# Optimization experiments

Measured on AMD Instinct MI355X. Metric: run time of the kernel, lower is better.

## Reference

```python
import jax, jax.numpy as jnp
import numpy as np

N = 64
DX0 = np.pi / N
B = 4096
N_ENV = 8
CODE = 128


def setup_inputs() -> dict:
    key = jax.random.key(0)
    k1, k2, k3 = jax.random.split(key, 3)
    y0 = jax.random.normal(k1, (B, 1, N, N), dtype=jnp.float32)
    env = jax.random.randint(k2, (B,), 0, N_ENV).astype(jnp.int64)
    codes = jax.random.normal(k3, (B, CODE), dtype=jnp.float32)
    t = jnp.zeros((1,), dtype=jnp.float32)
    # learned params: [mu, domain_placeholder] per env (matches nn.Parameter init)
    params = jnp.concatenate([jnp.full((N_ENV, 1), 0.005, jnp.float32),
                              jnp.full((N_ENV, 1), 1.0, jnp.float32)], axis=1)
    # fixed domain buffer for n_env == 8
    domain = jnp.array([0.75, 1.0, 0.75, 1.0, 0.75, 1.0, 0.75, 1.0],
                       dtype=jnp.float32)[:, None]  # [n_env, 1]
    return {"t": t, "y0": y0, "env": env, "codes": codes,
            "params": params, "domain": domain}


def _dx(a):  # roll along last axis (torch dims=2 on [B,H,W])
    return jnp.roll(a, -1, axis=2) - jnp.roll(a, 1, axis=2)


def _dy(a):  # roll along axis 1
    return jnp.roll(a, -1, axis=1) - jnp.roll(a, 1, axis=1)


def _laplacian2d(a, fdx2):
    # torch conv2d (cross-correlation) with kernel [[0,1,0],[1,-4,1],[1,1,0]]
    # and circular padding; note the asymmetric bottom row (faithful to source).
    lap = (jnp.roll(a, 1, axis=1)                    # a[i-1, j]
           + jnp.roll(a, 1, axis=2)                  # a[i, j-1]
           - 4.0 * a
           + jnp.roll(a, -1, axis=2)                 # a[i, j+1]
           + jnp.roll(jnp.roll(a, -1, axis=1), 1, axis=2)  # a[i+1, j-1]
           + jnp.roll(a, -1, axis=1))                # a[i+1, j]
    return lap / fdx2


def _poisson_solve(w, fdx):
    # w: [B,N,N]; fdx: [B,1] grid spacing per sample
    w_pad = jnp.pad(w, ((0, 0), (0, 1), (0, 1)), mode='wrap')  # [B,N+1,N+1]
    wf = jnp.fft.fft2(w_pad / (N ** 2))
    base = jnp.fft.fftfreq(N + 1).astype(w.dtype)       # fftfreq(n, d) = base / d
    k = (2.0 * np.pi) * base[None, :] / fdx             # [B, N+1]
    k2 = k[:, :, None] ** 2 + k[:, None, :] ** 2        # [B, N+1, N+1]
    uf = -wf / (1e-12 + k2)
    uf = uf.at[:, 0, 0].set(0.0)
    return jnp.fft.ifft2((N ** 2) * uf).real[:, :N, :N]


def reference(t, y0, env, codes, params, domain):
    x = y0[:, 0]                              # [B,N,N]
    p = params[env]                           # [B,2]
    mu = p[:, 0:1][..., None]                 # [B,1,1]
    fdx = domain[env] * DX0                   # [B,1]
    psi = _poisson_solve(-x, fdx)             # [B,N,N]
    fdx2 = (fdx[..., None]) ** 2              # [B,1,1]

    rxm = jnp.roll(x, -1, axis=2); rxp = jnp.roll(x, 1, axis=2)
    rym = jnp.roll(x, -1, axis=1); ryp = jnp.roll(x, 1, axis=1)
    pxm = jnp.roll(psi, -1, axis=2); pxp = jnp.roll(psi, 1, axis=2)
    pym = jnp.roll(psi, -1, axis=1); pyp = jnp.roll(psi, 1, axis=1)

    J1 = (_dy(psi) * _dx(x) - _dx(psi) * _dy(x)) / (4.0 * fdx2)
    J2 = (rxm * _dy(pxm) - rxp * _dy(pxp)
          - rym * _dx(pym) + ryp * _dx(pyp)) / (4.0 * fdx2)
    J3 = (jnp.roll(rxm, -1, axis=1) * (pym - pxm)
          - jnp.roll(rxp, 1, axis=1) * (pxp - pyp)
          - jnp.roll(rxp, -1, axis=1) * (pym - pxp)
          + jnp.roll(rxm, 1, axis=1) * (pxm - pyp)) / (4.0 * fdx2)

    dudt = -(J1 + J2 + J3) / 3.0 + mu * _laplacian2d(x, fdx2)
    return dudt[:, None]                      # [B,1,N,N]
```

## Files before the change

kernel.cpp:

```cpp
#include <hip/hip_runtime.h>
#include <math.h>


typedef _Float16 half8 __attribute__((ext_vector_type(8)));
typedef _Float16 half4 __attribute__((ext_vector_type(4)));
typedef float floatx4 __attribute__((ext_vector_type(4)));

#define WPI 0.09666439165562847f

#define H_TB1 0
#define H_TA2 10240
#define H_TG  20480
#define H_TH  26624
#define F_GR32 16384
#define F_GI32 16432
#define F_HC32 16480
#define F_HS32 16528
#define F_SE   16576
#define F_SEG  (F_SE + 264)

#define ARENA 40448
#define NB 2
#define OFF_YT   0
#define OFF_XR   0
#define OFF_XI   9216
#define OFF_X32R 18432
#define OFF_X32I 18688
#define OFF_ST   18944
#define OFF_S32  37952
#define OFF_PSIT 18944

__device__ __forceinline__ float trig65(int t, int isSin) {
    return isSin ? __sinf(WPI * (float)t) : __cosf(WPI * (float)t);
}

__global__ void setup_tables(float* __restrict__ ws, const float* __restrict__ domain) {
    int idx = blockIdx.x * 256 + threadIdx.x;
    _Float16* tbH = (_Float16*)ws;
    const float inv = 1.0f / 4225.0f;
    if (idx < 32768) {
        float v = 0.0f;
        int part;
        if (idx < 10240) {
            int chunk = idx >> 9, within = idx & 511;
            part = chunk & 1; int kc = (chunk >> 1) & 1, ni = chunk >> 2;
            int l2 = within >> 3, j = within & 7;
            int row = 16 * ni + (l2 & 15);
            int k = 32 * kc + 8 * (l2 >> 4) + j;
            if (row < 66) {
                int c = (row < 32) ? row : (row < 64 ? row - 32 : 32);
                int isS = (row < 32) ? 0 : (row < 64 ? 1 : row - 64);
                v = trig65((k * c) % 65, isS);
                if (k == 0) v += trig65((64 * c) % 65, isS);
            }
        } else if (idx < 20480) {
            int i2 = idx - 10240;
            int chunk = i2 >> 9, within = i2 & 511;
            part = chunk & 1; int kc = (chunk >> 1) & 1, mi = chunk >> 2;
            int l2 = within >> 3, j = within & 7;
            int row = 16 * mi + (l2 & 15);
            int m = 32 * kc + 8 * (l2 >> 4) + j;
            if (row < 66) {
                int jr = (row < 32) ? row : (row < 64 ? row - 32 : 32);
                int isS = (row < 32) ? 0 : (row < 64 ? 1 : row - 64);
                float s = isS ? 1.0f : -1.0f;
                v = s * trig65((jr * m) % 65, isS);
                if (m == 0) v += s * trig65((jr * 64) % 65, isS);
            }
        } else if (idx < 26624) {
            int i2 = idx - 20480;
            int chunk = i2 >> 9, within = i2 & 511;
            part = chunk & 1; int g = (chunk >> 1) & 1, si = chunk >> 2;
            int l2 = within >> 3, j = within & 7;
            int s = 16 * si + (l2 & 15);
            int jj = 8 * (l2 >> 4) + j;
            if (s <= 32) v = trig65((s * jj) % 65, g);
        } else {
            int i2 = idx - 26624;
            int chunk = i2 >> 9, within = i2 & 511;
            part = chunk & 1; int h = (chunk >> 1) & 1, pi2 = chunk >> 2;
            int l2 = within >> 3, j = within & 7;
            int p = 16 * pi2 + (l2 & 15);
            int c = 8 * (l2 >> 4) + j;
            if (p <= 32) {
                if (c == 0) v = h ? 0.0f : inv;
                else v = 2.0f * inv * trig65((c * p) % 65, h);
            }
        }
        _Float16 hh = (_Float16)v;
        tbH[idx] = part ? (_Float16)(v - (float)hh) : hh;
    } else if (idx < 32960) {
        int i2 = idx - 32768;
        int grp = i2 / 48, s = i2 - grp * 48;
        float v = 0.0f;
        if (s <= 32) {
            int t = (32 * s) % 65;
            float cs = __cosf(WPI * t), sn = __sinf(WPI * t);
            v = (grp == 0) ? cs : (grp == 1) ? sn : (grp == 2) ? 2.0f * inv * cs : 2.0f * inv * sn;
        }
        ws[F_GR32 + i2] = v;
    } else if (idx < 41672) {
        int i2 = idx - 32960;
        const float DX0 = 0.04908738521234052f;
        int e2, a, b2;
        if (i2 < 264) { e2 = i2 / 33; a = i2 - e2 * 33; b2 = 32; }
        else {
            int i3 = i2 - 264;
            e2 = i3 / 1056;
            int rem = i3 - e2 * 1056;
            a = rem >> 5; b2 = rem & 31;
        }
        float fdx = domain[e2] * DX0;
        float tt = 6.283185307179586f / (65.0f * fdx);
        float s2v = tt * tt;
        ws[F_SE + i2] = -1.0f / (1e-12f + s2v * (float)(a * a + b2 * b2));
    }
}

#define MFMA16(A, B, C) __builtin_amdgcn_mfma_f32_16x16x32_f16((A), (B), (C), 0, 0, 0)

__global__ __launch_bounds__(1024, 4)
void turb_kernel(const float* __restrict__ y0, const int* __restrict__ env,
                 const float* __restrict__ params, const float* __restrict__ domain,
                 const float* __restrict__ ws, float* __restrict__ out) {
    __shared__ __align__(16) char lds_raw[NB * ARENA];

    const int b0 = blockIdx.x * NB, tid = threadIdx.x;
    const int wid = __builtin_amdgcn_readfirstlane(tid >> 6);
    const int lane = tid & 63, n16 = lane & 15, q = lane >> 4;
    const int lane8 = lane * 8;
    const _Float16* tbH = (const _Float16*)ws;
    const float* tf = ws;

    int eA[NB];
    const float *SegA[NB], *Se3A[NB], *xA[NB];
    float* outA[NB];
    float invfA[NB], inv12A[NB];
    const float DX0 = 0.04908738521234052f;
    #pragma unroll
    for (int t = 0; t < NB; t++) {
        eA[t] = __builtin_amdgcn_readfirstlane(env[b0 + t]);
        SegA[t] = tf + F_SEG + eA[t] * 1056;
        Se3A[t] = tf + F_SE + eA[t] * 33;
        xA[t]   = y0 + (size_t)(b0 + t) * 4096;
        outA[t] = out + (size_t)(b0 + t) * 4096;
        float mu = params[2 * eA[t]];
        float f = domain[eA[t]] * DX0, f2 = f * f;
        inv12A[t] = 1.0f / (12.0f * f2);
        invfA[t] = mu / f2;
    }

    {
        const int mi = wid & 3;
        const int g1 = wid >> 2;
        half8 Ah[NB][2], Al[NB][2];
        #pragma unroll
        for (int t = 0; t < NB; t++) {
            const float* xrow = xA[t] + (16 * mi + n16) * 64 + 8 * q;
            #pragma unroll
            for (int kc = 0; kc < 2; kc++) {
                float4 v0 = *(const float4*)(xrow + 32 * kc);
                float4 v1 = *(const float4*)(xrow + 32 * kc + 4);
                float vv[8] = {v0.x, v0.y, v0.z, v0.w, v1.x, v1.y, v1.z, v1.w};
                #pragma unroll
                for (int u = 0; u < 8; u++) {
                    _Float16 h = (_Float16)vv[u];
                    Ah[t][kc][u] = h; Al[t][kc][u] = (_Float16)(vv[u] - (float)h);
                }
            }
        }
        const int niBeg = (g1 == 0) ? 0 : g1 + 1;
        const int niEnd = (g1 == 0) ? 2 : g1 + 2;
        for (int ni = niBeg; ni < niEnd; ni++) {
            const _Float16* tb = tbH + H_TB1 + ni * 2048 + lane8;
            half8 B0h = *(const half8*)(tb);
            half8 B0l = *(const half8*)(tb + 512);
            half8 B1h = *(const half8*)(tb + 1024);
            half8 B1l = *(const half8*)(tb + 1536);
            const int cp = 16 * ni + n16;
            const bool st = (ni < 4 || n16 < 2);
            #pragma unroll
            for (int t = 0; t < NB; t++) {
                floatx4 acc = {0.f, 0.f, 0.f, 0.f};
                acc = MFMA16(Ah[t][0], B0h, acc); acc = MFMA16(Ah[t][0], B0l, acc); acc = MFMA16(Al[t][0], B0h, acc);
                acc = MFMA16(Ah[t][1], B1h, acc); acc = MFMA16(Ah[t][1], B1l, acc); acc = MFMA16(Al[t][1], B1h, acc);
                if (st) {
                    half4 hh, ll;
                    #pragma unroll
                    for (int i = 0; i < 4; i++) {
                        _Float16 h = (_Float16)acc[i];
                        hh[i] = h; ll[i] = (_Float16)(acc[i] - (float)h);
                    }
                    _Float16* Yt = (_Float16*)(lds_raw + t * ARENA + OFF_YT);
                    *(half4*)(Yt + cp * 136 + 16 * mi + 4 * q) = hh;
                    *(half4*)(Yt + cp * 136 + 64 + 16 * mi + 4 * q) = ll;
                }
            }
        }
    }
    __syncthreads();

    for (int pos = wid; pos < 25; pos += 16) {
        const int mi = pos / 5, ni = pos - 5 * mi;
        const _Float16* ta = tbH + H_TA2 + mi * 2048 + lane8;
        half8 Ah0 = *(const half8*)(ta);
        half8 Al0 = *(const half8*)(ta + 512);
        half8 Ah1 = *(const half8*)(ta + 1024);
        half8 Al1 = *(const half8*)(ta + 1536);
        const int yoff = (16 * ni + n16) * 136 + 8 * q;
        const int cp = 16 * ni + n16;
        const int cc = (ni == 4) ? 32 : (cp & 31);
        const int isS = (ni == 4) ? n16 : (ni >> 1);
        const bool valid = (ni < 4) || (n16 < 2);
        #pragma unroll
        for (int t = 0; t < NB; t++) {
            const _Float16* Yt = (const _Float16*)(lds_raw + t * ARENA + OFF_YT);
            const _Float16* yrow = Yt + yoff;
            half8 Bh0 = *(const half8*)(yrow);
            half8 Bl0 = *(const half8*)(yrow + 64);
            half8 Bh1 = *(const half8*)(yrow + 32);
            half8 Bl1 = *(const half8*)(yrow + 96);
            floatx4 acc = {0.f, 0.f, 0.f, 0.f};
            acc = MFMA16(Ah0, Bh0, acc); acc = MFMA16(Ah0, Bl0, acc); acc = MFMA16(Al0, Bh0, acc);
            acc = MFMA16(Ah1, Bh1, acc); acc = MFMA16(Ah1, Bl1, acc); acc = MFMA16(Al1, Bh1, acc);
            if (valid) {
                _Float16* ST = (_Float16*)(lds_raw + t * ARENA + OFF_ST);
                float* S32 = (float*)(lds_raw + t * ARENA + OFF_S32);
                if (mi < 4) {
                    const int isQ = mi >> 1;
                    const int sid = isQ ? (isS ? 3 : 1) : (isS ? 2 : 0);
                    const int jjb = 16 * (mi & 1) + 4 * q;
                    floatx4 Sv = *(const floatx4*)(SegA[t] + cc * 32 + jjb);
                    float ssg = (sid == 2) ? -2.0f : 2.0f;
                    half4 hh, ll;
                    #pragma unroll
                    for (int i = 0; i < 4; i++) {
                        float v = ssg * Sv[i] * acc[i];
                        _Float16 h = (_Float16)v;
                        hh[i] = h; ll[i] = (_Float16)(v - (float)h);
                    }
                    _Float16* sb = ST + sid * 2376 + cc * 72 + jjb;
                    *(half4*)sb = hh;
                    *(half4*)(sb + 32) = ll;
                } else if (q == 0) {
                    float S = Se3A[t][cc];
                    #pragma unroll
                    for (int i = 0; i < 2; i++) {
                        int sid = i ? (isS ? 3 : 1) : (isS ? 2 : 0);
                        float v = 2.0f * S * acc[i];
                        if (sid == 2) v = -v;
                        S32[sid * 36 + cc] = v;
                    }
                }
            }
        }
    }
    __syncthreads();

    if (wid < NB && lane < 33) {
        _Float16* ST = (_Float16*)(lds_raw + wid * ARENA + OFF_ST);
        const int c = lane;
        float v0[4];
        #pragma unroll
        for (int sid = 0; sid < 4; sid++)
            v0[sid] = (float)ST[sid * 2376 + c * 72] + (float)ST[sid * 2376 + c * 72 + 32];
        float pr = 0.5f * (v0[0] + v0[3]), pi = 0.5f * (v0[1] + v0[2]);
        if (c == 0) { pr = 0.f; pi = 0.f; }
        float outs[4] = {pr, pi, pi, pr};
        #pragma unroll
        for (int sid = 0; sid < 4; sid++) {
            _Float16 h = (_Float16)outs[sid];
            ST[sid * 2376 + c * 72] = h;
            ST[sid * 2376 + c * 72 + 32] = (_Float16)(outs[sid] - (float)h);
        }
    }
    __syncthreads();

    for (int pos = wid; pos < 18; pos += 16) {
        const int ci = pos / 6, rem = pos - 6 * ci;
        const int si = rem >> 1, g = rem & 1;
        const _Float16* tg = tbH + H_TG + si * 2048 + lane8;
        half8 Grh = *(const half8*)(tg);
        half8 Grl = *(const half8*)(tg + 512);
        half8 Gih = *(const half8*)(tg + 1024);
        half8 Gil = *(const half8*)(tg + 1536);
        const int s = 16 * si + n16;
        const float ga = tf[F_GR32 + s], gi2 = tf[F_GI32 + s];
        const bool sval = (si < 2) || (n16 == 0);
        const float sgn = g ? 1.0f : -1.0f;
        const int cb = 16 * ci + 4 * q;
        const int aoff = (2 * g) * 2376 + (16 * ci + n16) * 72 + 8 * q;
        #pragma unroll
        for (int t = 0; t < NB; t++) {
            const _Float16* ST = (const _Float16*)(lds_raw + t * ARENA + OFF_ST);
            const float* S32 = (const float*)(lds_raw + t * ARENA + OFF_S32);
            const _Float16* st0 = ST + aoff;
            half8 A0h = *(const half8*)(st0),        A0l = *(const half8*)(st0 + 32);
            half8 A1h = *(const half8*)(st0 + 2376), A1l = *(const half8*)(st0 + 2376 + 32);
            floatx4 aA = {0.f,0.f,0.f,0.f}, aB = aA;
            aA = MFMA16(A0h, Grh, aA); aA = MFMA16(A0h, Grl, aA); aA = MFMA16(A0l, Grh, aA);
            aB = MFMA16(A1h, Gih, aB); aB = MFMA16(A1h, Gil, aB); aB = MFMA16(A1l, Gih, aB);
            _Float16* Xo = (_Float16*)(lds_raw + t * ARENA + (g ? OFF_XI : OFF_XR));
            float* X32o = (float*)(lds_raw + t * ARENA + (g ? OFF_X32I : OFF_X32R));
            if (ci < 2) {
                floatx4 U0 = *(const floatx4*)(S32 + (2 * g) * 36 + cb);
                floatx4 U1 = *(const floatx4*)(S32 + (2 * g + 1) * 36 + cb);
                half4 hP, lP, hM, lM;
                #pragma unroll
                for (int i = 0; i < 4; i++) {
                    float av = aA[i] + ga * U0[i], bv = aB[i] + gi2 * U1[i];
                    float xP = av + sgn * bv;
                    float xM = av - sgn * bv;
                    _Float16 h;
                    h = (_Float16)xP; hP[i] = h; lP[i] = (_Float16)(xP - (float)h);
                    h = (_Float16)xM; hM[i] = h; lM[i] = (_Float16)(xM - (float)h);
                }
                if (sval) {
                    *(half4*)(Xo + s * 72 + cb) = hP;  *(half4*)(Xo + s * 72 + 32 + cb) = lP;
                    if (s >= 2) {
                        int sm = 65 - s;
                        *(half4*)(Xo + sm * 72 + cb) = hM;  *(half4*)(Xo + sm * 72 + 32 + cb) = lM;
                    }
                }
            } else if (q == 0 && sval) {
                float u0 = S32[(2 * g) * 36 + 32], u1 = S32[(2 * g + 1) * 36 + 32];
                float av = aA[0] + ga * u0, bv = aB[0] + gi2 * u1;
                X32o[s] = av + sgn * bv;
                if (s >= 2) X32o[65 - s] = av - sgn * bv;
            }
        }
    }
    __syncthreads();

    for (int p24 = wid; p24 < 24; p24 += 16) {
        const int t = p24 / 12;
        const int pos = p24 - 12 * t;
        const int ri = pos / 3, pti = pos - 3 * ri;
        const char* base = lds_raw + t * ARENA;
        const _Float16* Xr = (const _Float16*)(base + OFF_XR);
        const _Float16* Xi = (const _Float16*)(base + OFF_XI);
        const float* X32r = (const float*)(base + OFF_X32R);
        const float* X32i = (const float*)(base + OFF_X32I);
        float* psiT = (float*)(base + OFF_PSIT);
        const int brow = (16 * ri + n16) * 72 + 8 * q;
        half8 Brh = *(const half8*)(Xr + brow), Brl = *(const half8*)(Xr + brow + 32);
        half8 Bih = *(const half8*)(Xi + brow), Bil = *(const half8*)(Xi + brow + 32);
        const _Float16* th = tbH + H_TH + pti * 2048 + lane8;
        half8 Hch = *(const half8*)(th);
        half8 Hcl = *(const half8*)(th + 512);
        half8 Hsh = *(const half8*)(th + 1024);
        half8 Hsl = *(const half8*)(th + 1536);
        floatx4 aE = {0.f,0.f,0.f,0.f}, aF = aE;
        aE = MFMA16(Hch, Brh, aE); aE = MFMA16(Hch, Brl, aE); aE = MFMA16(Hcl, Brh, aE);
        aF = MFMA16(Hsh, Bih, aF); aF = MFMA16(Hsh, Bil, aF); aF = MFMA16(Hsl, Bih, aF);
        const int r = 16 * ri + n16;
        float xr32 = X32r[r], xi32 = X32i[r];
        if (pti < 2) {
            const int pb = 16 * pti + 4 * q;
            floatx4 Hc4 = *(const floatx4*)(tf + F_HC32 + pb);
            floatx4 Hs4 = *(const floatx4*)(tf + F_HS32 + pb);
            float* pp = psiT + pb * 65 + r;
            float* pm = psiT + (65 - pb) * 65 + r;
            #pragma unroll
            for (int i = 0; i < 4; i++) {
                float E = aE[i] + xr32 * Hc4[i];
                float F = aF[i] + xi32 * Hs4[i];
                pp[i * 65] = E - F;
                if (pb + i >= 2) pm[-i * 65] = E + F;
            }
        } else if (q == 0) {
            float E = aE[0] + xr32 * tf[F_HC32 + 32];
            float F = aF[0] + xi32 * tf[F_HS32 + 32];
            psiT[32 * 65 + r] = E - F;
            psiT[33 * 65 + r] = E + F;
        }
    }
    __syncthreads();

    #pragma unroll
    for (int t = 0; t < NB; t++) {
        const float* psiT = (const float*)(lds_raw + t * ARENA + OFF_PSIT);
        const float* x0 = xA[t];
        const float inv12 = inv12A[t], invf = invfA[t];
        const int c = lane;
        const int cm1 = (c + 63) & 63, cp1 = (c + 1) & 63;
        const int r0 = wid * 4;
        const float* xL = x0 + r0 * 64 + cm1;
        const float* xC = x0 + r0 * 64 + c;
        const float* xR = x0 + r0 * 64 + cp1;
        const float* pL = psiT + cm1 * 65 + r0;
        const float* pC = psiT + c * 65 + r0;
        const float* pR = psiT + cp1 * 65 + r0;
        float* ob = outA[t] + r0 * 64 + c;
        const int mo = (wid == 0) ? 63 : -1;
        float xLm = xL[mo * 64], xCm = xC[mo * 64], xRm = xR[mo * 64];
        float pLm = pL[mo], pCm = pC[mo], pRm = pR[mo];
        float xLc = xL[0], xCc = xC[0], xRc = xR[0];
        float pLc = pL[0], pCc = pC[0], pRc = pR[0];
        #pragma unroll
        for (int it = 0; it < 4; it++) {
            int ro = it + 1;
            if (it == 3 && wid == 15) ro = -60;
            float xLp = xL[ro * 64], xCp = xC[ro * 64], xRp = xR[ro * 64];
            float pLp = pL[ro], pCp = pC[ro], pRp = pR[ro];
            float J1 = (pCp - pCm) * (xRc - xLc) - (pRc - pLc) * (xCp - xCm);
            float J2 = xRc * (pRp - pRm) - xLc * (pLp - pLm) - xCp * (pRp - pLp) + xCm * (pRm - pLm);
            float J3 = xRp * (pCp - pRc) - xLm * (pLc - pCm) - xLp * (pCp - pLc) + xRm * (pRc - pCm);
            float lap = xCm + xLc - 4.f * xCc + xRc + xLp + xCp;
            ob[it * 64] = -(J1 + J2 + J3) * inv12 + lap * invf;
            xLm = xLc; xCm = xCc; xRm = xRc; pLm = pLc; pCm = pCc; pRm = pRc;
            xLc = xLp; xCc = xCp; xRc = xRp; pLc = pLp; pCc = pCp; pRc = pRp;
        }
    }
}

extern "C" void kernel_launch(void* const* d_in, const int* in_sizes, int n_in,
                              void* d_out, int out_size, void* d_ws, size_t ws_size,
                              hipStream_t stream) {
    const float* y0     = (const float*)d_in[1];
    const int*   env    = (const int*)d_in[2];
    const float* params = (const float*)d_in[4];
    const float* domain = (const float*)d_in[5];
    float* out = (float*)d_out;
    float* ws  = (float*)d_ws;

    setup_tables<<<dim3(163), dim3(256), 0, stream>>>(ws, domain);
    turb_kernel<<<dim3(2048), dim3(1024), 0, stream>>>(y0, env, params, domain, ws, out);
}
```

Baseline: 203.4 us.

## Halve block to 512 threads, rebalance stage work, fold DC fixup into GEMM

```diff
diff --git a/kernel.cpp b/kernel.cpp
--- a/kernel.cpp
+++ b/kernel.cpp
@@ -119,7 +119,7 @@
 
 #define MFMA16(A, B, C) __builtin_amdgcn_mfma_f32_16x16x32_f16((A), (B), (C), 0, 0, 0)
 
-__global__ __launch_bounds__(1024, 4)
+__global__ __launch_bounds__(512, 2)
 void turb_kernel(const float* __restrict__ y0, const int* __restrict__ env,
                  const float* __restrict__ params, const float* __restrict__ domain,
                  const float* __restrict__ ws, float* __restrict__ out) {
@@ -152,7 +152,7 @@
 
     {
         const int mi = wid & 3;
-        const int g1 = wid >> 2;
+        const int hi = wid >> 2;
         half8 Ah[NB][2], Al[NB][2];
         #pragma unroll
         for (int t = 0; t < NB; t++) {
@@ -169,51 +169,61 @@
                 }
             }
         }
-        const int niBeg = (g1 == 0) ? 0 : g1 + 1;
-        const int niEnd = (g1 == 0) ? 2 : g1 + 2;
-        for (int ni = niBeg; ni < niEnd; ni++) {
+        half8 B0h, B0l, B1h, B1l;
+        int cp; bool st;
+        auto s1_pos = [&](int ni) {
             const _Float16* tb = tbH + H_TB1 + ni * 2048 + lane8;
-            half8 B0h = *(const half8*)(tb);
-            half8 B0l = *(const half8*)(tb + 512);
-            half8 B1h = *(const half8*)(tb + 1024);
-            half8 B1l = *(const half8*)(tb + 1536);
-            const int cp = 16 * ni + n16;
-            const bool st = (ni < 4 || n16 < 2);
-            #pragma unroll
-            for (int t = 0; t < NB; t++) {
-                floatx4 acc = {0.f, 0.f, 0.f, 0.f};
-                acc = MFMA16(Ah[t][0], B0h, acc); acc = MFMA16(Ah[t][0], B0l, acc); acc = MFMA16(Al[t][0], B0h, acc);
-                acc = MFMA16(Ah[t][1], B1h, acc); acc = MFMA16(Ah[t][1], B1l, acc); acc = MFMA16(Al[t][1], B1h, acc);
-                if (st) {
-                    half4 hh, ll;
-                    #pragma unroll
-                    for (int i = 0; i < 4; i++) {
-                        _Float16 h = (_Float16)acc[i];
-                        hh[i] = h; ll[i] = (_Float16)(acc[i] - (float)h);
-                    }
-                    _Float16* Yt = (_Float16*)(lds_raw + t * ARENA + OFF_YT);
-                    *(half4*)(Yt + cp * 136 + 16 * mi + 4 * q) = hh;
-                    *(half4*)(Yt + cp * 136 + 64 + 16 * mi + 4 * q) = ll;
+            B0h = *(const half8*)(tb);
+            B0l = *(const half8*)(tb + 512);
+            B1h = *(const half8*)(tb + 1024);
+            B1l = *(const half8*)(tb + 1536);
+            cp = 16 * ni + n16;
+            st = (ni < 4 || n16 < 2);
+        };
+        auto s1_body = [&](int t) {
+            floatx4 acc = {0.f, 0.f, 0.f, 0.f};
+            acc = MFMA16(Ah[t][0], B0h, acc); acc = MFMA16(Ah[t][0], B0l, acc); acc = MFMA16(Al[t][0], B0h, acc);
+            acc = MFMA16(Ah[t][1], B1h, acc); acc = MFMA16(Ah[t][1], B1l, acc); acc = MFMA16(Al[t][1], B1h, acc);
+            if (st) {
+                half4 hh, ll;
+                #pragma unroll
+                for (int i = 0; i < 4; i++) {
+                    _Float16 h = (_Float16)acc[i];
+                    hh[i] = h; ll[i] = (_Float16)(acc[i] - (float)h);
                 }
-            }
-        }
+                _Float16* Yt = (_Float16*)(lds_raw + t * ARENA + OFF_YT);
+                *(half4*)(Yt + cp * 136 + 16 * mi + 4 * q) = hh;
+                *(half4*)(Yt + cp * 136 + 64 + 16 * mi + 4 * q) = ll;
+            }
+        };
+        const int niBeg = hi ? 3 : 0;
+        #pragma unroll
+        for (int kk = 0; kk < 2; kk++) {
+            s1_pos(niBeg + kk);
+            s1_body(0); s1_body(1);
+        }
+        s1_pos(2);
+        s1_body(hi);
     }
     __syncthreads();
 
-    for (int pos = wid; pos < 25; pos += 16) {
-        const int mi = pos / 5, ni = pos - 5 * mi;
-        const _Float16* ta = tbH + H_TA2 + mi * 2048 + lane8;
-        half8 Ah0 = *(const half8*)(ta);
-        half8 Al0 = *(const half8*)(ta + 512);
-        half8 Ah1 = *(const half8*)(ta + 1024);
-        half8 Al1 = *(const half8*)(ta + 1536);
-        const int yoff = (16 * ni + n16) * 136 + 8 * q;
-        const int cp = 16 * ni + n16;
-        const int cc = (ni == 4) ? 32 : (cp & 31);
-        const int isS = (ni == 4) ? n16 : (ni >> 1);
-        const bool valid = (ni < 4) || (n16 < 2);
-        #pragma unroll
-        for (int t = 0; t < NB; t++) {
+    {
+        half8 Ah0, Al0, Ah1, Al1;
+        int mi, ni, cc, isS, yoff; bool valid;
+        auto s2_pos = [&](int pos) {
+            mi = pos / 5; ni = pos - 5 * mi;
+            const _Float16* ta = tbH + H_TA2 + mi * 2048 + lane8;
+            Ah0 = *(const half8*)(ta);
+            Al0 = *(const half8*)(ta + 512);
+            Ah1 = *(const half8*)(ta + 1024);
+            Al1 = *(const half8*)(ta + 1536);
+            yoff = (16 * ni + n16) * 136 + 8 * q;
+            int cp = 16 * ni + n16;
+            cc = (ni == 4) ? 32 : (cp & 31);
+            isS = (ni == 4) ? n16 : (ni >> 1);
+            valid = (ni < 4) || (n16 < 2);
+        };
+        auto s2_body = [&](int t) {
             const _Float16* Yt = (const _Float16*)(lds_raw + t * ARENA + OFF_YT);
             const _Float16* yrow = Yt + yoff;
             half8 Bh0 = *(const half8*)(yrow);
@@ -253,50 +263,59 @@
                     }
                 }
             }
+        };
+        #pragma unroll
+        for (int k = 0; k < 3; k++) {
+            s2_pos(wid + 8 * k);
+            s2_body(0); s2_body(1);
+        }
+        if (wid < 2) {
+            s2_pos(24);
+            s2_body(wid);
         }
     }
     __syncthreads();
 
-    if (wid < NB && lane < 33) {
-        _Float16* ST = (_Float16*)(lds_raw + wid * ARENA + OFF_ST);
-        const int c = lane;
-        float v0[4];
-        #pragma unroll
-        for (int sid = 0; sid < 4; sid++)
-            v0[sid] = (float)ST[sid * 2376 + c * 72] + (float)ST[sid * 2376 + c * 72 + 32];
-        float pr = 0.5f * (v0[0] + v0[3]), pi = 0.5f * (v0[1] + v0[2]);
-        if (c == 0) { pr = 0.f; pi = 0.f; }
-        float outs[4] = {pr, pi, pi, pr};
-        #pragma unroll
-        for (int sid = 0; sid < 4; sid++) {
-            _Float16 h = (_Float16)outs[sid];
-            ST[sid * 2376 + c * 72] = h;
-            ST[sid * 2376 + c * 72 + 32] = (_Float16)(outs[sid] - (float)h);
-        }
-    }
-    __syncthreads();
-
-    for (int pos = wid; pos < 18; pos += 16) {
-        const int ci = pos / 6, rem = pos - 6 * ci;
-        const int si = rem >> 1, g = rem & 1;
-        const _Float16* tg = tbH + H_TG + si * 2048 + lane8;
-        half8 Grh = *(const half8*)(tg);
-        half8 Grl = *(const half8*)(tg + 512);
-        half8 Gih = *(const half8*)(tg + 1024);
-        half8 Gil = *(const half8*)(tg + 1536);
-        const int s = 16 * si + n16;
-        const float ga = tf[F_GR32 + s], gi2 = tf[F_GI32 + s];
-        const bool sval = (si < 2) || (n16 == 0);
-        const float sgn = g ? 1.0f : -1.0f;
-        const int cb = 16 * ci + 4 * q;
-        const int aoff = (2 * g) * 2376 + (16 * ci + n16) * 72 + 8 * q;
-        #pragma unroll
-        for (int t = 0; t < NB; t++) {
+    {
+        half8 Grh, Grl, Gih, Gil;
+        int ci, si, g, s, cb, aoff; float ga, gi2, sgn; bool sval;
+        auto s4a_pos = [&](int pos) {
+            ci = pos / 6; int rem = pos - 6 * ci;
+            si = rem >> 1; g = rem & 1;
+            const _Float16* tg = tbH + H_TG + si * 2048 + lane8;
+            Grh = *(const half8*)(tg);
+            Grl = *(const half8*)(tg + 512);
+            Gih = *(const half8*)(tg + 1024);
+            Gil = *(const half8*)(tg + 1536);
+            s = 16 * si + n16;
+            ga = tf[F_GR32 + s]; gi2 = tf[F_GI32 + s];
+            sval = (si < 2) || (n16 == 0);
+            sgn = g ? 1.0f : -1.0f;
+            cb = 16 * ci + 4 * q;
+            aoff = (2 * g) * 2376 + (16 * ci + n16) * 72 + 8 * q;
+        };
+        auto s4a_body = [&](int t) {
             const _Float16* ST = (const _Float16*)(lds_raw + t * ARENA + OFF_ST);
             const float* S32 = (const float*)(lds_raw + t * ARENA + OFF_S32);
             const _Float16* st0 = ST + aoff;
             half8 A0h = *(const half8*)(st0),        A0l = *(const half8*)(st0 + 32);
             half8 A1h = *(const half8*)(st0 + 2376), A1l = *(const half8*)(st0 + 2376 + 32);
+            if (q == 0) {
+                const int cA = 16 * ci + n16;
+                const int co = cA * 72;
+                float v0 = (float)ST[co]            + (float)ST[co + 32];
+                float v1 = (float)ST[2376 + co]     + (float)ST[2376 + co + 32];
+                float v2 = (float)ST[4752 + co]     + (float)ST[4752 + co + 32];
+                float v3 = (float)ST[7128 + co]     + (float)ST[7128 + co + 32];
+                float pr = 0.5f * (v0 + v3), pi = 0.5f * (v1 + v2);
+                if (cA == 0) { pr = 0.f; pi = 0.f; }
+                float w0 = g ? pi : pr;
+                float w1 = g ? pr : pi;
+                _Float16 h0 = (_Float16)w0;
+                A0h[0] = h0; A0l[0] = (_Float16)(w0 - (float)h0);
+                _Float16 h1 = (_Float16)w1;
+                A1h[0] = h1; A1l[0] = (_Float16)(w1 - (float)h1);
+            }
             floatx4 aA = {0.f,0.f,0.f,0.f}, aB = aA;
             aA = MFMA16(A0h, Grh, aA); aA = MFMA16(A0h, Grl, aA); aA = MFMA16(A0l, Grh, aA);
             aB = MFMA16(A1h, Gih, aB); aB = MFMA16(A1h, Gil, aB); aB = MFMA16(A1l, Gih, aB);
@@ -328,11 +347,20 @@
                 X32o[s] = av + sgn * bv;
                 if (s >= 2) X32o[65 - s] = av - sgn * bv;
             }
+        };
+        #pragma unroll
+        for (int k = 0; k < 2; k++) {
+            s4a_pos(wid + 8 * k);
+            s4a_body(0); s4a_body(1);
+        }
+        if (wid < 4) {
+            s4a_pos(16 + (wid >> 1));
+            s4a_body(wid & 1);
         }
     }
     __syncthreads();
 
-    for (int p24 = wid; p24 < 24; p24 += 16) {
+    for (int p24 = wid; p24 < 24; p24 += 8) {
         const int t = p24 / 12;
         const int pos = p24 - 12 * t;
         const int ri = pos / 3, pti = pos - 3 * ri;
@@ -384,7 +412,7 @@
         const float inv12 = inv12A[t], invf = invfA[t];
         const int c = lane;
         const int cm1 = (c + 63) & 63, cp1 = (c + 1) & 63;
-        const int r0 = wid * 4;
+        const int r0 = wid * 8;
         const float* xL = x0 + r0 * 64 + cm1;
         const float* xC = x0 + r0 * 64 + c;
         const float* xR = x0 + r0 * 64 + cp1;
@@ -398,9 +426,9 @@
         float xLc = xL[0], xCc = xC[0], xRc = xR[0];
         float pLc = pL[0], pCc = pC[0], pRc = pR[0];
         #pragma unroll
-        for (int it = 0; it < 4; it++) {
+        for (int it = 0; it < 8; it++) {
             int ro = it + 1;
-            if (it == 3 && wid == 15) ro = -60;
+            if (it == 7 && wid == 7) ro = -56;
             float xLp = xL[ro * 64], xCp = xC[ro * 64], xRp = xR[ro * 64];
             float pLp = pL[ro], pCp = pC[ro], pRp = pR[ro];
             float J1 = (pCp - pCm) * (xRc - xLc) - (pRc - pLc) * (xCp - xCm);
@@ -425,5 +453,5 @@
     float* ws  = (float*)d_ws;
 
     setup_tables<<<dim3(163), dim3(256), 0, stream>>>(ws, domain);
-    turb_kernel<<<dim3(2048), dim3(1024), 0, stream>>>(y0, env, params, domain, ws, out);
+    turb_kernel<<<dim3(2048), dim3(512), 0, stream>>>(y0, env, params, domain, ws, out);
 }
```

Result: faster. 198.8 us (-2.3%).
